# Performance work log

Hardware: AMD Instinct MI355X
Metric: run time of the kernel (lower is better)

The kernel has to match this reference:

```python
import jax, jax.numpy as jnp
import numpy as np

EMBED_DIM = 1024
HEAD_DIM = 64


def setup_inputs() -> dict:
    key = jax.random.key(0)
    ks = jax.random.split(key, 7)
    s_in = EMBED_DIM ** -0.5  # torch Linear default init scale
    x = jax.random.normal(ks[0], (4, 4096, EMBED_DIM), dtype=jnp.float32)
    Wk = jax.random.uniform(ks[1], (HEAD_DIM, EMBED_DIM), jnp.float32, -s_in, s_in)
    bk = jax.random.uniform(ks[2], (HEAD_DIM,), jnp.float32, -s_in, s_in)
    Wq = jax.random.uniform(ks[3], (HEAD_DIM, EMBED_DIM), jnp.float32, -s_in, s_in)
    bq = jax.random.uniform(ks[4], (HEAD_DIM,), jnp.float32, -s_in, s_in)
    Wv = jax.random.uniform(ks[5], (HEAD_DIM, EMBED_DIM), jnp.float32, -s_in, s_in)
    bv = jax.random.uniform(ks[6], (HEAD_DIM,), jnp.float32, -s_in, s_in)
    return {"x": x, "Wq": Wq, "bq": bq, "Wk": Wk, "bk": bk, "Wv": Wv, "bv": bv}


def reference(x, Wq, bq, Wk, bk, Wv, bv):
    # torch Linear: y = x @ W.T + b
    q = jnp.einsum('btc,dc->btd', x, Wq) + bq  # [B,T,D]
    k = jnp.einsum('btc,dc->btd', x, Wk) + bk
    v = jnp.einsum('btc,dc->btd', x, Wv) + bv
    scale = HEAD_DIM ** -0.5
    # NOTE: original divides by scale (multiplies by sqrt(head_dim)) -- faithful
    scores = jnp.einsum('btd,bsd->bts', q, k) / scale  # [B,T,T]
    attn_weights = jax.nn.softmax(scores, axis=-1)
    return jnp.einsum('bts,bsd->btd', attn_weights, v)
```

## Files before the change

### kernel.cpp

```cpp
#include <hip/hip_runtime.h>

#define BATCH 4
#define SEQ   4096
#define CDIM  1024
#define DDIM  64
#define NROW  (BATCH * SEQ)
#define NSPL  8

typedef _Float16 f16;
typedef _Float16 f16x8 __attribute__((ext_vector_type(8)));
typedef _Float16 f16x4 __attribute__((ext_vector_type(4)));
typedef __fp16   h16x2 __attribute__((ext_vector_type(2)));
typedef float    f32x4 __attribute__((ext_vector_type(4)));

#define MFMA32(a, b, c) __builtin_amdgcn_mfma_f32_16x16x32_f16((a), (b), (c), 0, 0, 0)
#define MFMA16(a, b, c) __builtin_amdgcn_mfma_f32_16x16x16f16((a), (b), (c), 0, 0, 0)

#define GLDS(g, l)                                                            \
  __builtin_amdgcn_global_load_lds((const __attribute__((address_space(1))) void*)(g), \
                                   (__attribute__((address_space(3))) void*)(l), 16, 0, 0)

#define QSCALE 11.5415603f

__device__ inline f16x8 cvt8(f32x4 a, f32x4 b) {
  h16x2 p0 = __builtin_amdgcn_cvt_pkrtz(a[0], a[1]);
  h16x2 p1 = __builtin_amdgcn_cvt_pkrtz(a[2], a[3]);
  h16x2 p2 = __builtin_amdgcn_cvt_pkrtz(b[0], b[1]);
  h16x2 p3 = __builtin_amdgcn_cvt_pkrtz(b[2], b[3]);
  f16x8 r;
  r[0] = p0[0]; r[1] = p0[1]; r[2] = p1[0]; r[3] = p1[1];
  r[4] = p2[0]; r[5] = p2[1]; r[6] = p3[0]; r[7] = p3[1];
  return r;
}

__device__ inline f16x4 cvt4(float a, float b, float c, float d) {
  h16x2 lo = __builtin_amdgcn_cvt_pkrtz(a, b);
  h16x2 hi = __builtin_amdgcn_cvt_pkrtz(c, d);
  f16x4 r;
  r[0] = lo[0]; r[1] = lo[1]; r[2] = hi[0]; r[3] = hi[1];
  return r;
}

__global__ __launch_bounds__(256) void prep_w_kernel(const float* __restrict__ Wq,
                                                     const float* __restrict__ Wk,
                                                     const float* __restrict__ Wv,
                                                     f16* __restrict__ wf2) {
  const int t = blockIdx.x * 256 + threadIdx.x;
  const int lane = t & 63;
  const int s = t >> 6;
  const int mt = s % 12, ck = s / 12;
  const int mat = mt >> 2, tile = mt & 3;
  const int n = lane & 15, quad = lane >> 4;
  const float* W = (mat == 0) ? Wq : (mat == 1) ? Wk : Wv;
  const float* src = W + (size_t)(tile * 16 + n) * CDIM + ck * 32 + quad * 8;
  const f32x4 a = *(const f32x4*)src;
  const f32x4 b = *(const f32x4*)(src + 4);
  *(f16x8*)(wf2 + (size_t)t * 8) = cvt8(a, b);
}

__global__ __launch_bounds__(512, 4) void proj_kernel(const float* __restrict__ x,
                                                      const f16* __restrict__ wf2,
                                                      const float* __restrict__ bq,
                                                      const float* __restrict__ bk,
                                                      const float* __restrict__ bv,
                                                      f16* __restrict__ qs,
                                                      f16* __restrict__ ks,
                                                      f16* __restrict__ vc) {
  __shared__ __attribute__((aligned(16))) char pbuf[2][16384];
  const int tid = threadIdx.x, lane = tid & 63, w = tid >> 6;
  const int n = lane & 15, quad = lane >> 4;
  const int rw = w & 1, wc = w >> 1;
  const int rowbase = blockIdx.x * 32;

  const int i0 = 2 * w;
  const float* xs0 = x + (size_t)(rowbase + i0 * 8 + (lane >> 3)) * CDIM + (lane & 7) * 4;
  const float* xs1 = xs0 + 8 * CDIM;
  const int wi = (i0 >= 4) ? (i0 - 4) : 0;
  const f16* ws0 = wf2 + (size_t)wi * 512 + lane * 8;
  const f16* ws1 = ws0 + 512;

  f32x4 acc[3];
#pragma unroll
  for (int i = 0; i < 3; ++i) acc[i] = (f32x4){0.f, 0.f, 0.f, 0.f};

  auto issue = [&](int ck, int buf) {
    char* base = &pbuf[buf][0];
    if (i0 < 4) {
      GLDS(xs0 + ck * 32, base + i0 * 1024);
      GLDS(xs1 + ck * 32, base + (i0 + 1) * 1024);
    } else {
      GLDS(ws0 + (size_t)ck * 6144, base + 4096 + (i0 - 4) * 1024);
      GLDS(ws1 + (size_t)ck * 6144, base + 4096 + (i0 - 3) * 1024);
    }
  };

  issue(0, 0);
  for (int ck = 0; ck < 32; ++ck) {
    const int b = ck & 1;
    __syncthreads();
    if (ck + 1 < 32) issue(ck + 1, b ^ 1);
    const float* xb = (const float*)&pbuf[b][0];
    const f16* wb = (const f16*)&pbuf[b][4096];
    const f32x4 x0 = *(const f32x4*)(xb + (rw * 16 + n) * 32 + quad * 8);
    const f32x4 x1 = *(const f32x4*)(xb + (rw * 16 + n) * 32 + quad * 8 + 4);
    const f16x8 a = cvt8(x0, x1);
#pragma unroll
    for (int i = 0; i < 3; ++i) {
      const f16x8 bf = *(const f16x8*)(wb + (wc * 3 + i) * 512 + lane * 8);
      acc[i] = MFMA32(a, bf, acc[i]);
    }
  }

  const float* bias_p[3] = {bq, bk, bv};
#pragma unroll
  for (int i = 0; i < 3; ++i) {
    const int mt = wc * 3 + i;
    const int mat = mt >> 2, tile = mt & 3;
    const int d = tile * 16 + n;
    const float bias = bias_p[mat][d];
    const int r0 = rowbase + rw * 16 + quad * 4;
    const f32x4 aa = acc[i];
    if (mat == 0) {
#pragma unroll
      for (int r = 0; r < 4; ++r)
        qs[(size_t)(r0 + r) * DDIM + d] = (f16)((aa[r] + bias) * QSCALE);
    } else if (mat == 1) {
#pragma unroll
      for (int r = 0; r < 4; ++r) {
        const int t = r0 + r;
        const int col = ((((d >> 3) ^ (t & 7)) << 3) | (n & 7));
        ks[(size_t)t * DDIM + col] = (f16)(aa[r] + bias);
      }
    } else {
      const int bb = r0 >> 12;
      const int tl = r0 & (SEQ - 1);
      const int ck2 = tl >> 6;
      const int bsw = (((tl & 63) >> 2) ^ n) << 2;
      *(f16x4*)(vc + ((size_t)(bb * 64 + ck2) * 64 + d) * 64 + bsw) =
          cvt4(aa[0] + bias, aa[1] + bias, aa[2] + bias, aa[3] + bias);
    }
  }
}

template <int NSPLIT>
__global__ __launch_bounds__(256, 4) void attn_kernel(const f16* __restrict__ qs,
                                                      const f16* __restrict__ ks,
                                                      const f16* __restrict__ vc,
                                                      float* __restrict__ outp,
                                                      f16* __restrict__ pacc,
                                                      float* __restrict__ pm,
                                                      float* __restrict__ pl) {
  __shared__ __attribute__((aligned(16))) f16 lk[2][4096];
  __shared__ __attribute__((aligned(16))) f16 lv[2][4096];
  const int tid = threadIdx.x, lane = tid & 63, w = tid >> 6;
  const int n = lane & 15, quad = lane >> 4;
  const int split = blockIdx.x % NSPLIT;
  const int rowblk = blockIdx.x / NSPLIT;
  const int row0 = rowblk * 128 + w * 32;
  const int bb = row0 >> 12;
  const int kbase = split * (SEQ / NSPLIT);
  const int kc0 = kbase >> 6;
  const int NC = SEQ / NSPLIT / 64;

  const f16* ksb = ks + (size_t)bb * SEQ * DDIM;
  const f16* vcb = vc + (size_t)bb * 64 * 4096;

  auto issue = [&](int c, int buf) {
#pragma unroll
    for (int i = 0; i < 2; ++i) {
      const int id = 2 * w + i;
      GLDS(ksb + (size_t)(kbase + c * 64) * 64 + id * 512 + lane * 8, &lk[buf][id * 512]);
      GLDS(vcb + (size_t)(kc0 + c) * 4096 + id * 512 + lane * 8, &lv[buf][id * 512]);
    }
  };

  f16x8 qf[2][2];
#pragma unroll
  for (int g = 0; g < 2; ++g)
#pragma unroll
    for (int hh = 0; hh < 2; ++hh)
      qf[g][hh] = *(const f16x8*)(qs + (size_t)(row0 + g * 16 + n) * DDIM + hh * 32 + quad * 8);

  const int kswz = (quad ^ (n & 7)) << 3;
  int vswz[4];
#pragma unroll
  for (int st = 0; st < 4; ++st) vswz[st] = ((((st << 2) | quad) ^ n) << 2);

  f32x4 acc[2][4];
  float m[2] = {-1e30f, -1e30f}, ll[2] = {0.f, 0.f};
#pragma unroll
  for (int g = 0; g < 2; ++g)
#pragma unroll
    for (int t = 0; t < 4; ++t) acc[g][t] = (f32x4){0.f, 0.f, 0.f, 0.f};

  issue(0, 0);
  for (int c = 0; c < NC; ++c) {
    const int b = c & 1;
    __syncthreads();
    if (c + 1 < NC) issue(c + 1, b ^ 1);

    f32x4 s[2][4];
#pragma unroll
    for (int st = 0; st < 4; ++st) {
      const f16* lkr = &lk[b][(st * 16 + n) * 64];
      const f16x8 klo = *(const f16x8*)(lkr + kswz);
      const f16x8 khi = *(const f16x8*)(lkr + (kswz ^ 32));
#pragma unroll
      for (int g = 0; g < 2; ++g) {
        f32x4 z = (f32x4){0.f, 0.f, 0.f, 0.f};
        z = MFMA32(klo, qf[g][0], z);
        s[g][st] = MFMA32(khi, qf[g][1], z);
      }
    }

    f16x4 pq[2][4];
#pragma unroll
    for (int g = 0; g < 2; ++g) {
      f32x4 mx;
#pragma unroll
      for (int r = 0; r < 4; ++r)
        mx[r] = fmaxf(fmaxf(s[g][0][r], s[g][1][r]), fmaxf(s[g][2][r], s[g][3][r]));
      float mloc = fmaxf(fmaxf(mx[0], mx[1]), fmaxf(mx[2], mx[3]));
      mloc = fmaxf(mloc, __shfl_xor(mloc, 16));
      mloc = fmaxf(mloc, __shfl_xor(mloc, 32));
      const float mnew = fmaxf(m[g], mloc);
      const float alpha = __builtin_amdgcn_exp2f(m[g] - mnew);
      m[g] = mnew;
      float psum = 0.f;
#pragma unroll
      for (int st = 0; st < 4; ++st) {
        f32x4 p;
#pragma unroll
        for (int r = 0; r < 4; ++r) p[r] = __builtin_amdgcn_exp2f(s[g][st][r] - mnew);
        psum += (p[0] + p[1]) + (p[2] + p[3]);
        pq[g][st] = cvt4(p[0], p[1], p[2], p[3]);
      }
      ll[g] = ll[g] * alpha + psum;
#pragma unroll
      for (int t = 0; t < 4; ++t) acc[g][t] *= alpha;
    }

#pragma unroll
    for (int dt = 0; dt < 4; ++dt) {
      const f16* lvr = &lv[b][(dt * 16 + n) * 64];
#pragma unroll
      for (int st = 0; st < 4; ++st) {
        const f16x4 va = *(const f16x4*)(lvr + vswz[st]);
        acc[0][dt] = MFMA16(va, pq[0][st], acc[0][dt]);
        acc[1][dt] = MFMA16(va, pq[1][st], acc[1][dt]);
      }
    }
  }

  float lred[2];
#pragma unroll
  for (int g = 0; g < 2; ++g) {
    float l = ll[g];
    l += __shfl_xor(l, 16);
    l += __shfl_xor(l, 32);
    lred[g] = l;
  }

  if (NSPLIT == 1) {
#pragma unroll
    for (int g = 0; g < 2; ++g) {
      const float inv = 1.0f / lred[g];
      const int q = row0 + g * 16 + n;
#pragma unroll
      for (int t = 0; t < 4; ++t) {
        f32x4 o = acc[g][t];
#pragma unroll
        for (int r = 0; r < 4; ++r) o[r] *= inv;
        *(f32x4*)(outp + (size_t)q * DDIM + t * 16 + quad * 4) = o;
      }
    }
  } else {
#pragma unroll
    for (int g = 0; g < 2; ++g) {
      const int q = row0 + g * 16 + n;
#pragma unroll
      for (int t = 0; t < 4; ++t)
        *(f16x4*)(pacc + ((size_t)split * NROW + q) * DDIM + t * 16 + quad * 4) =
            cvt4(acc[g][t][0], acc[g][t][1], acc[g][t][2], acc[g][t][3]);
      if (quad == 0) {
        pm[split * NROW + q] = m[g];
        pl[split * NROW + q] = lred[g];
      }
    }
  }
}

template <int NSPLIT>
__global__ __launch_bounds__(256) void combine_kernel(const f16* __restrict__ pacc,
                                                      const float* __restrict__ pm,
                                                      const float* __restrict__ pl,
                                                      float* __restrict__ out) {
  const int idx = blockIdx.x * 256 + threadIdx.x;
  const int row = idx >> 4;
  const int c = (idx & 15) * 4;
  float mm = pm[row];
#pragma unroll
  for (int s = 1; s < NSPLIT; ++s) mm = fmaxf(mm, pm[s * NROW + row]);
  float L = 0.f;
  f32x4 o = (f32x4){0.f, 0.f, 0.f, 0.f};
#pragma unroll
  for (int s = 0; s < NSPLIT; ++s) {
    const float e = __builtin_amdgcn_exp2f(pm[s * NROW + row] - mm);
    L += pl[s * NROW + row] * e;
    const f16x4 a = *(const f16x4*)(pacc + ((size_t)s * NROW + row) * DDIM + c);
#pragma unroll
    for (int j = 0; j < 4; ++j) o[j] += (float)a[j] * e;
  }
  const float inv = 1.0f / L;
#pragma unroll
  for (int j = 0; j < 4; ++j) o[j] *= inv;
  *(f32x4*)(out + (size_t)row * DDIM + c) = o;
}

extern "C" void kernel_launch(void* const* d_in, const int* in_sizes, int n_in,
                              void* d_out, int out_size, void* d_ws, size_t ws_size,
                              hipStream_t stream) {
  const float* x  = (const float*)d_in[0];
  const float* Wq = (const float*)d_in[1];
  const float* bq = (const float*)d_in[2];
  const float* Wk = (const float*)d_in[3];
  const float* bk = (const float*)d_in[4];
  const float* Wv = (const float*)d_in[5];
  const float* bv = (const float*)d_in[6];
  float* out = (float*)d_out;

  f16* wf2 = (f16*)d_ws;
  f16* qs = wf2 + 3 * 65536;
  f16* ks = qs + (size_t)NROW * DDIM;
  f16* vc = ks + (size_t)NROW * DDIM;
  f16* pacc = vc + (size_t)NROW * DDIM;
  float* pm = (float*)(pacc + (size_t)NSPL * NROW * DDIM);
  float* pl = pm + (size_t)NSPL * NROW;
  const size_t need = (size_t)((char*)(pl + (size_t)NSPL * NROW) - (char*)d_ws);

  prep_w_kernel<<<dim3(96), dim3(256), 0, stream>>>(Wq, Wk, Wv, wf2);
  proj_kernel<<<dim3(512), dim3(512), 0, stream>>>(x, wf2, bq, bk, bv, qs, ks, vc);

  if (ws_size >= need) {
    attn_kernel<NSPL><<<dim3(128 * NSPL), dim3(256), 0, stream>>>(qs, ks, vc, nullptr, pacc, pm, pl);
    combine_kernel<NSPL><<<dim3(NROW * 16 / 256), dim3(256), 0, stream>>>(pacc, pm, pl, out);
  } else {
    attn_kernel<1><<<dim3(128), dim3(256), 0, stream>>>(qs, ks, vc, out, nullptr, nullptr, nullptr);
  }
}
```

Baseline: 161.8 us.

## Split QKV projection over K dimension with partial sums and combine kernel

Restructures the projection GEMM so each block handles 64 rows and one quarter of the 1024-wide reduction. Each block writes fp16 partial results to a workspace, and a new combine kernel sums the four partials, adds bias, applies the Q scale and writes Q/K/V in their swizzled layouts. Each block also computes a larger register tile (2 row tiles by 6 column tiles), so every loaded fragment feeds more MFMAs. The aim is more parallelism and better operand reuse; the cost is an extra kernel launch, extra workspace traffic, and fp16 rounding of the partial sums.

After: 159.6 us. Within noise of the previous version (-1.3%).

```diff
diff --git a/kernel.cpp b/kernel.cpp
--- a/kernel.cpp
+++ b/kernel.cpp
@@ -6,6 +6,8 @@
 #define DDIM  64
 #define NROW  (BATCH * SEQ)
 #define NSPL  8
+#define KS    4
+#define SEG   (NROW * DDIM)
 
 typedef _Float16 f16;
 typedef _Float16 f16x8 __attribute__((ext_vector_type(8)));
@@ -58,87 +60,138 @@
   *(f16x8*)(wf2 + (size_t)t * 8) = cvt8(a, b);
 }
 
-__global__ __launch_bounds__(512, 4) void proj_kernel(const float* __restrict__ x,
+__global__ __launch_bounds__(256, 4) void proj_kernel(const float* __restrict__ x,
                                                       const f16* __restrict__ wf2,
-                                                      const float* __restrict__ bq,
-                                                      const float* __restrict__ bk,
-                                                      const float* __restrict__ bv,
-                                                      f16* __restrict__ qs,
-                                                      f16* __restrict__ ks,
-                                                      f16* __restrict__ vc) {
-  __shared__ __attribute__((aligned(16))) char pbuf[2][16384];
+                                                      f16* __restrict__ ppart) {
+  __shared__ __attribute__((aligned(16))) char smem[2][20480];
   const int tid = threadIdx.x, lane = tid & 63, w = tid >> 6;
   const int n = lane & 15, quad = lane >> 4;
   const int rw = w & 1, wc = w >> 1;
-  const int rowbase = blockIdx.x * 32;
-
-  const int i0 = 2 * w;
-  const float* xs0 = x + (size_t)(rowbase + i0 * 8 + (lane >> 3)) * CDIM + (lane & 7) * 4;
-  const float* xs1 = xs0 + 8 * CDIM;
-  const int wi = (i0 >= 4) ? (i0 - 4) : 0;
-  const f16* ws0 = wf2 + (size_t)wi * 512 + lane * 8;
-  const f16* ws1 = ws0 + 512;
-
-  f32x4 acc[3];
-#pragma unroll
-  for (int i = 0; i < 3; ++i) acc[i] = (f32x4){0.f, 0.f, 0.f, 0.f};
-
-  auto issue = [&](int ck, int buf) {
-    char* base = &pbuf[buf][0];
-    if (i0 < 4) {
-      GLDS(xs0 + ck * 32, base + i0 * 1024);
-      GLDS(xs1 + ck * 32, base + (i0 + 1) * 1024);
-    } else {
-      GLDS(ws0 + (size_t)ck * 6144, base + 4096 + (i0 - 4) * 1024);
-      GLDS(ws1 + (size_t)ck * 6144, base + 4096 + (i0 - 3) * 1024);
-    }
+  const int rowblk = blockIdx.x >> 2, split = blockIdx.x & 3;
+  const int rowbase = rowblk * 64;
+
+  const float* xsrc[2];
+#pragma unroll
+  for (int j = 0; j < 2; ++j) {
+    const int i = 2 * w + j;
+    xsrc[j] = x + (size_t)(rowbase + i * 8 + (lane >> 3)) * CDIM + split * 256 + (lane & 7) * 4;
+  }
+  const f16* wsrc[3];
+#pragma unroll
+  for (int j = 0; j < 3; ++j) {
+    const int mt = 3 * w + j;
+    wsrc[j] = wf2 + (size_t)(split * 96 + mt) * 512 + lane * 8;
+  }
+
+  f32x4 acc[2][6];
+#pragma unroll
+  for (int rt = 0; rt < 2; ++rt)
+#pragma unroll
+    for (int i = 0; i < 6; ++i) acc[rt][i] = (f32x4){0.f, 0.f, 0.f, 0.f};
+
+  auto issue = [&](int ck, int b) {
+    char* base = &smem[b][0];
+#pragma unroll
+    for (int j = 0; j < 2; ++j)
+      GLDS(xsrc[j] + ck * 32, base + (2 * w + j) * 1024);
+#pragma unroll
+    for (int j = 0; j < 3; ++j)
+      GLDS(wsrc[j] + (size_t)ck * 6144, base + 8192 + (3 * w + j) * 1024);
   };
 
   issue(0, 0);
-  for (int ck = 0; ck < 32; ++ck) {
+  for (int ck = 0; ck < 8; ++ck) {
     const int b = ck & 1;
     __syncthreads();
-    if (ck + 1 < 32) issue(ck + 1, b ^ 1);
-    const float* xb = (const float*)&pbuf[b][0];
-    const f16* wb = (const f16*)&pbuf[b][4096];
-    const f32x4 x0 = *(const f32x4*)(xb + (rw * 16 + n) * 32 + quad * 8);
-    const f32x4 x1 = *(const f32x4*)(xb + (rw * 16 + n) * 32 + quad * 8 + 4);
-    const f16x8 a = cvt8(x0, x1);
-#pragma unroll
-    for (int i = 0; i < 3; ++i) {
-      const f16x8 bf = *(const f16x8*)(wb + (wc * 3 + i) * 512 + lane * 8);
-      acc[i] = MFMA32(a, bf, acc[i]);
-    }
-  }
-
-  const float* bias_p[3] = {bq, bk, bv};
-#pragma unroll
-  for (int i = 0; i < 3; ++i) {
-    const int mt = wc * 3 + i;
+    if (ck + 1 < 8) issue(ck + 1, b ^ 1);
+    const char* base = &smem[b][0];
+    f16x8 a[2];
+#pragma unroll
+    for (int rt = 0; rt < 2; ++rt) {
+      const int i = rw * 4 + rt * 2 + (n >> 3);
+      const float* xp = (const float*)(base + i * 1024 + (n & 7) * 128 + quad * 32);
+      a[rt] = cvt8(*(const f32x4*)xp, *(const f32x4*)(xp + 4));
+    }
+#pragma unroll
+    for (int i2 = 0; i2 < 6; ++i2) {
+      const f16x8 bf = *(const f16x8*)(base + 8192 + (wc * 6 + i2) * 1024 + lane * 16);
+      acc[0][i2] = MFMA32(a[0], bf, acc[0][i2]);
+      acc[1][i2] = MFMA32(a[1], bf, acc[1][i2]);
+    }
+  }
+
+#pragma unroll
+  for (int i2 = 0; i2 < 6; ++i2) {
+    const int mt = wc * 6 + i2;
     const int mat = mt >> 2, tile = mt & 3;
     const int d = tile * 16 + n;
-    const float bias = bias_p[mat][d];
-    const int r0 = rowbase + rw * 16 + quad * 4;
-    const f32x4 aa = acc[i];
-    if (mat == 0) {
-#pragma unroll
-      for (int r = 0; r < 4; ++r)
-        qs[(size_t)(r0 + r) * DDIM + d] = (f16)((aa[r] + bias) * QSCALE);
-    } else if (mat == 1) {
-#pragma unroll
-      for (int r = 0; r < 4; ++r) {
-        const int t = r0 + r;
-        const int col = ((((d >> 3) ^ (t & 7)) << 3) | (n & 7));
-        ks[(size_t)t * DDIM + col] = (f16)(aa[r] + bias);
-      }
-    } else {
-      const int bb = r0 >> 12;
-      const int tl = r0 & (SEQ - 1);
-      const int ck2 = tl >> 6;
-      const int bsw = (((tl & 63) >> 2) ^ n) << 2;
-      *(f16x4*)(vc + ((size_t)(bb * 64 + ck2) * 64 + d) * 64 + bsw) =
-          cvt4(aa[0] + bias, aa[1] + bias, aa[2] + bias, aa[3] + bias);
-    }
+    f16* seg = ppart + ((size_t)mat * KS + split) * SEG;
+#pragma unroll
+    for (int rt = 0; rt < 2; ++rt) {
+      const int r0 = rowbase + rw * 32 + rt * 16 + quad * 4;
+      const f32x4 aa = acc[rt][i2];
+      if (mat == 0) {
+#pragma unroll
+        for (int r = 0; r < 4; ++r)
+          seg[(size_t)(r0 + r) * DDIM + d] = (f16)aa[r];
+      } else if (mat == 1) {
+#pragma unroll
+        for (int r = 0; r < 4; ++r) {
+          const int t = r0 + r;
+          const int col = ((((d >> 3) ^ (t & 7)) << 3) | (d & 7));
+          seg[(size_t)t * DDIM + col] = (f16)aa[r];
+        }
+      } else {
+        const int bb = r0 >> 12;
+        const int tl = r0 & (SEQ - 1);
+        const int ck2 = tl >> 6;
+        const int bsw = (((tl & 63) >> 2) ^ n) << 2;
+        *(f16x4*)(seg + ((size_t)(bb * 64 + ck2) * 64 + d) * 64 + bsw) =
+            cvt4(aa[0], aa[1], aa[2], aa[3]);
+      }
+    }
+  }
+}
+
+__global__ __launch_bounds__(256) void combine_proj_kernel(const f16* __restrict__ ppart,
+                                                           const float* __restrict__ bq,
+                                                           const float* __restrict__ bk,
+                                                           const float* __restrict__ bv,
+                                                           f16* __restrict__ qs,
+                                                           f16* __restrict__ ks,
+                                                           f16* __restrict__ vc) {
+  const int seg = blockIdx.x / 512;
+  const int tix = (blockIdx.x - seg * 512) * 256 + threadIdx.x;
+  const size_t base = (size_t)tix * 8;
+  const f16* pp = ppart + (size_t)seg * KS * SEG + base;
+
+  float s[8];
+#pragma unroll
+  for (int j = 0; j < 8; ++j) s[j] = 0.f;
+#pragma unroll
+  for (int sp = 0; sp < KS; ++sp) {
+    const f16x8 v = *(const f16x8*)(pp + (size_t)sp * SEG);
+#pragma unroll
+    for (int j = 0; j < 8; ++j) s[j] += (float)v[j];
+  }
+
+  f16x8 o;
+  if (seg == 0) {
+    const int d0 = (int)(base & 63);
+#pragma unroll
+    for (int j = 0; j < 8; ++j) o[j] = (f16)((s[j] + bq[d0 + j]) * QSCALE);
+    *(f16x8*)(qs + base) = o;
+  } else if (seg == 1) {
+    const int t = (int)(base >> 6);
+    const int d0 = (((int)(base & 63) >> 3) ^ (t & 7)) << 3;
+#pragma unroll
+    for (int j = 0; j < 8; ++j) o[j] = (f16)(s[j] + bk[d0 + j]);
+    *(f16x8*)(ks + base) = o;
+  } else {
+    const float b = bv[(int)(base >> 6) & 63];
+#pragma unroll
+    for (int j = 0; j < 8; ++j) o[j] = (f16)(s[j] + b);
+    *(f16x8*)(vc + base) = o;
   }
 }
 
@@ -331,15 +384,17 @@
 
   f16* wf2 = (f16*)d_ws;
   f16* qs = wf2 + 3 * 65536;
-  f16* ks = qs + (size_t)NROW * DDIM;
-  f16* vc = ks + (size_t)NROW * DDIM;
-  f16* pacc = vc + (size_t)NROW * DDIM;
-  float* pm = (float*)(pacc + (size_t)NSPL * NROW * DDIM);
+  f16* ks = qs + (size_t)SEG;
+  f16* vc = ks + (size_t)SEG;
+  f16* ppart = vc + (size_t)SEG;
+  f16* pacc = ppart + (size_t)3 * KS * SEG;
+  float* pm = (float*)(pacc + (size_t)NSPL * SEG);
   float* pl = pm + (size_t)NSPL * NROW;
   const size_t need = (size_t)((char*)(pl + (size_t)NSPL * NROW) - (char*)d_ws);
 
   prep_w_kernel<<<dim3(96), dim3(256), 0, stream>>>(Wq, Wk, Wv, wf2);
-  proj_kernel<<<dim3(512), dim3(512), 0, stream>>>(x, wf2, bq, bk, bv, qs, ks, vc);
+  proj_kernel<<<dim3(256 * KS), dim3(256), 0, stream>>>(x, wf2, ppart);
+  combine_proj_kernel<<<dim3(1536), dim3(256), 0, stream>>>(ppart, bq, bk, bv, qs, ks, vc);
 
   if (ws_size >= need) {
     attn_kernel<NSPL><<<dim3(128 * NSPL), dim3(256), 0, stream>>>(qs, ks, vc, nullptr, pacc, pm, pl);
```
